# Performance work log

Hardware: AMD Instinct MI355X
Metric: run time of the kernel (lower is better)

The kernel has to match this reference:

```python
import jax, jax.numpy as jnp
import numpy as np

B, C, H, W = 32, 256, 64, 64
LN_EPS = 1e-5

def _conv1x1(x, w, b=None):
    # x: (b,c,h,w), w: (out,c) -> (b,out,h,w)
    y = jnp.einsum('bchw,oc->bohw', x, w)
    if b is not None:
        y = y + b[None, :, None, None]
    return y

def _hsigmoid(t):
    # mmcv HSigmoid: clamp((x + 3) / 6, 0, 1)
    return jnp.clip((t + 3.0) / 6.0, 0.0, 1.0)

def setup_inputs() -> dict:
    key = jax.random.key(0)
    ks = jax.random.split(key, 12)
    s = 0.05
    return {
        'x': jax.random.normal(ks[0], (B, C, H, W), jnp.float32),
        'conv0_w': jax.random.normal(ks[1], (C // 2, C), jnp.float32) * s,
        'conv0_b': jnp.zeros((C // 2,), jnp.float32),
        'bn1_w': jax.random.normal(ks[2], (C, C // 2), jnp.float32) * s,
        'bn1_b': jnp.zeros((C,), jnp.float32),
        'conv1_w': jax.random.normal(ks[3], (1, C), jnp.float32) * s,
        'conv1_b': jnp.zeros((1,), jnp.float32),
        'ln_g': jnp.ones((C,), jnp.float32),
        'ln_b': jnp.zeros((C,), jnp.float32),
        'sk_w1': jax.random.normal(ks[4], (C // 2, C), jnp.float32) * s,
        'sk_w2': jax.random.normal(ks[5], (C, C // 2), jnp.float32) * s,
        'res_w': jax.random.normal(ks[6], (C, C), jnp.float32) * s,
        'res_b': jnp.zeros((C,), jnp.float32),
    }

def reference(x, conv0_w, conv0_b, bn1_w, bn1_b, conv1_w, conv1_b,
              ln_g, ln_b, sk_w1, sk_w2, res_w, res_b):
    b, c, h, w = x.shape
    # ---- channel attention ----
    ca = _conv1x1(x, conv0_w, conv0_b)               # (b, c/2, h, w)
    ca = ca.mean(axis=(2, 3), keepdims=True)          # GAP -> (b, c/2, 1, 1)
    ca = _conv1x1(ca, bn1_w, bn1_b)                   # (b, c, 1, 1)
    ca = _hsigmoid(ca)
    v = ca.reshape(b, c)                              # nchw_to_nlc -> (b, 1, c); LN over c
    mu = v.mean(axis=-1, keepdims=True)
    var = ((v - mu) ** 2).mean(axis=-1, keepdims=True)
    v = (v - mu) * jax.lax.rsqrt(var + LN_EPS) * ln_g + ln_b
    ca = v.reshape(b, c, 1, 1)
    # ---- spatial attention ----
    sa = _conv1x1(x, conv1_w, conv1_b)                # (b, 1, h, w)
    # ---- parallel attention ----
    par = _hsigmoid(sa + ca)                          # (b, c, h, w)
    # ---- sequence attention: bmm outer product (b,c,1)x(b,1,hw) ----
    seq = _hsigmoid(ca * sa)                          # (b, c, h, w)
    # ---- SK module ----
    u = (seq + par).mean(axis=(2, 3), keepdims=True)  # GAP -> (b, c, 1, 1)
    u = _conv1x1(u, sk_w1)                            # (b, c/2, 1, 1), no bias
    u = _conv1x1(u, sk_w2)                            # (b, c, 1, 1), no bias
    a = jax.nn.softmax(u, axis=1)
    sk = seq * a + par * (1.0 - a)
    # softmax over spatial (nchw_to_nlc + Softmax(dim=1))
    sk = jax.nn.softmax(sk.reshape(b, c, h * w), axis=2).reshape(b, c, h, w)
    selected = x * sk
    # ---- self attention ----
    self_attn = selected.sum(axis=(2, 3)).reshape(b, c, 1, 1) + _conv1x1(x, res_w, res_b)
    return selected + self_attn
```

## Files before the change

### kernel.cpp

```cpp
#include <hip/hip_runtime.h>
#include <math.h>

#define B_  32
#define C_  256
#define HW_ 4096
#define LN_EPS 1e-5f

typedef __attribute__((ext_vector_type(4))) float f32x4;
typedef __attribute__((ext_vector_type(8))) short bf16x8;
typedef __attribute__((ext_vector_type(4))) unsigned u32x4;
typedef __attribute__((ext_vector_type(2))) unsigned u32x2;

__device__ __forceinline__ float hsig(float v) {
    return fminf(fmaxf((v + 3.0f) * (1.0f / 6.0f), 0.0f), 1.0f);
}
__device__ __forceinline__ float tval(float ca, float a, float sav) {
    return a * hsig(ca * sav) + (1.0f - a) * hsig(ca + sav);
}
__device__ __forceinline__ unsigned short f2bf(float f) {
    unsigned u = __float_as_uint(f);
    unsigned r = (u + 0x7fffu + ((u >> 16) & 1u)) >> 16;
    return (unsigned short)r;
}
__device__ __forceinline__ float bf2f(unsigned short h) {
    return __uint_as_float(((unsigned)h) << 16);
}
__device__ __forceinline__ int bswz(int n) {
    return ((n & 7) ^ ((n >> 3) & 7)) << 4;
}


__global__ __launch_bounds__(1024) void k_pass1c(
    const float* __restrict__ x, const float* __restrict__ w1,
    float* __restrict__ sa, float* __restrict__ xs_part,
    unsigned short* __restrict__ xbf)
{
    __shared__ float sw1[C_];
    __shared__ float sred[16][256];
    __shared__ float xsl[C_];
    int hwq = blockIdx.x, b = blockIdx.y;
    int tid = threadIdx.x, w = tid >> 6, l = tid & 63;
    int hw0 = hwq * 256;
    if (tid < 256) sw1[tid] = w1[tid];
    __syncthreads();
    const float* xb = x + (size_t)b * (C_ * HW_) + hw0 + l * 4;
    unsigned short* xo = xbf + (size_t)b * (C_ * HW_) + hw0 + l * 4;
    f32x4 sacc = {0.f, 0.f, 0.f, 0.f};
    #pragma unroll 4
    for (int i = 0; i < 16; ++i) {
        int c = i * 16 + w;
        f32x4 v = *(const f32x4*)(xb + (size_t)c * HW_);
        sacc += sw1[c] * v;
        ushort4 o = { f2bf(v.x), f2bf(v.y), f2bf(v.z), f2bf(v.w) };
        *(ushort4*)(xo + (size_t)c * HW_) = o;
        float h = (v.x + v.y) + (v.z + v.w);
        h += __shfl_xor(h, 32); h += __shfl_xor(h, 16); h += __shfl_xor(h, 8);
        h += __shfl_xor(h, 4);  h += __shfl_xor(h, 2);  h += __shfl_xor(h, 1);
        if (l == 0) xsl[c] = h;
    }
    *(f32x4*)&sred[w][l * 4] = sacc;
    __syncthreads();
    if (tid < 256) {
        float s = 0.f;
        #pragma unroll
        for (int g = 0; g < 16; ++g) s += sred[g][tid];
        sa[(size_t)b * HW_ + hw0 + tid] = s;
        xs_part[((size_t)hwq * B_ + b) * C_ + tid] = xsl[tid];
    }
}

__global__ void k_ca(const float* __restrict__ xs_part, const float* __restrict__ w0,
                     const float* __restrict__ b0, const float* __restrict__ w1,
                     const float* __restrict__ b1, const float* __restrict__ g,
                     const float* __restrict__ be, float* __restrict__ ca,
                     const float* __restrict__ rw, unsigned short* __restrict__ wbs,
                     int nparts) {
    int b = blockIdx.x, tid = threadIdx.x;
    __shared__ float xm[C_], t0[128], red[4];
    float xs = 0.f;
    for (int i = 0; i < nparts; ++i)
        xs += xs_part[((size_t)i * B_ + b) * C_ + tid];
    xm[tid] = xs * (1.0f / HW_);
    __syncthreads();
    if (tid < 128) {
        float s = b0[tid];
        const float* wr = w0 + tid * C_;
        for (int c = 0; c < C_; ++c) s += wr[c] * xm[c];
        t0[tid] = s;
    }
    __syncthreads();
    float s = b1[tid];
    const float* wr = w1 + tid * 128;
    for (int o = 0; o < 128; ++o) s += wr[o] * t0[o];
    float v = hsig(s);
    float sum = v;
    #pragma unroll
    for (int o = 32; o; o >>= 1) sum += __shfl_xor(sum, o);
    if ((tid & 63) == 0) red[tid >> 6] = sum;
    __syncthreads();
    float mu = (red[0] + red[1] + red[2] + red[3]) * (1.0f / C_);
    __syncthreads();
    float d = v - mu;
    float sq = d * d;
    #pragma unroll
    for (int o = 32; o; o >>= 1) sq += __shfl_xor(sq, o);
    if ((tid & 63) == 0) red[tid >> 6] = sq;
    __syncthreads();
    float var = (red[0] + red[1] + red[2] + red[3]) * (1.0f / C_);
    ca[b * C_ + tid] = d * (1.0f / sqrtf(var + LN_EPS)) * g[tid] + be[tid];

    int gid = b * 256 + tid;
    int lane = gid & 63;
    int mi = (gid >> 6) & 3;
    int ks = (gid >> 8) & 7;
    int wv2 = gid >> 11;
    int m = wv2 * 64 + mi * 16 + (lane & 15);
    int kb = ks * 32 + (lane >> 4) * 8;
    const float* src = rw + m * C_ + kb;
    f32x4 a4 = *(const f32x4*)src;
    f32x4 b4 = *(const f32x4*)(src + 4);
    ushort4 o0 = { f2bf(a4.x), f2bf(a4.y), f2bf(a4.z), f2bf(a4.w) };
    ushort4 o1 = { f2bf(b4.x), f2bf(b4.y), f2bf(b4.z), f2bf(b4.w) };
    unsigned short* dst = wbs + (size_t)gid * 8;
    *(ushort4*)dst = o0;
    *(ushort4*)(dst + 4) = o1;
}

__global__ void k_u(const float* __restrict__ sa, const float* __restrict__ ca,
                    const float* __restrict__ b1, float* __restrict__ u) {
    int bc = blockIdx.x;
    int b = bc >> 8;
    int tid = threadIdx.x;
    float cav = ca[bc];
    float bias = b1[0];
    const float* sp = sa + (size_t)b * HW_;
    float s = 0.f;
    for (int i = 0; i < 16; ++i) {
        f32x4 v = *(const f32x4*)(sp + i * 256 + tid * 4);
        #pragma unroll
        for (int j = 0; j < 4; ++j) {
            float sv = v[j] + bias;
            s += hsig(cav * sv) + hsig(cav + sv);
        }
    }
    #pragma unroll
    for (int o = 32; o; o >>= 1) s += __shfl_xor(s, o);
    if (tid == 0) u[bc] = s * (1.0f / HW_);
}

__global__ void k_a(const float* __restrict__ u, const float* __restrict__ w1,
                    const float* __restrict__ w2, float* __restrict__ aout) {
    int b = blockIdx.x, tid = threadIdx.x;
    __shared__ float uu[C_], v0[128], red[4];
    uu[tid] = u[b * C_ + tid];
    __syncthreads();
    if (tid < 128) {
        float s = 0.f;
        const float* wr = w1 + tid * C_;
        for (int c = 0; c < C_; ++c) s += wr[c] * uu[c];
        v0[tid] = s;
    }
    __syncthreads();
    float s = 0.f;
    const float* wr = w2 + tid * 128;
    for (int o = 0; o < 128; ++o) s += wr[o] * v0[o];
    float m = s;
    #pragma unroll
    for (int o = 32; o; o >>= 1) m = fmaxf(m, __shfl_xor(m, o));
    if ((tid & 63) == 0) red[tid >> 6] = m;
    __syncthreads();
    m = fmaxf(fmaxf(red[0], red[1]), fmaxf(red[2], red[3]));
    __syncthreads();
    float e = __expf(s - m);
    float se = e;
    #pragma unroll
    for (int o = 32; o; o >>= 1) se += __shfl_xor(se, o);
    if ((tid & 63) == 0) red[tid >> 6] = se;
    __syncthreads();
    float tot = red[0] + red[1] + red[2] + red[3];
    aout[b * C_ + tid] = e / tot;
}

__global__ void k_stats3(const unsigned short* __restrict__ xbf, const float* __restrict__ sa,
                         const float* __restrict__ b1,
                         const float* __restrict__ ca, const float* __restrict__ aw,
                         const float* __restrict__ res_b, f32x4* __restrict__ st4) {
    int bc = blockIdx.x;
    int b = bc >> 8, c = bc & 255;
    int tid = threadIdx.x;
    float cav = ca[bc], av = aw[bc];
    float bias = b1[0];
    const float* sp = sa + (size_t)b * HW_;
    const unsigned* xp = (const unsigned*)(xbf + (size_t)bc * HW_);
    float se = 0.f, xe = 0.f;
    #pragma unroll
    for (int i = 0; i < 4; ++i) {
        f32x4 s4 = *(const f32x4*)(sp + i * 1024 + tid * 4);
        u32x2 x2 = *(const u32x2*)(xp + i * 512 + tid * 2);
        float xv[4];
        xv[0] = bf2f((unsigned short)(x2[0] & 0xffffu));
        xv[1] = bf2f((unsigned short)(x2[0] >> 16));
        xv[2] = bf2f((unsigned short)(x2[1] & 0xffffu));
        xv[3] = bf2f((unsigned short)(x2[1] >> 16));
        #pragma unroll
        for (int j = 0; j < 4; ++j) {
            float e = __expf(tval(cav, av, s4[j] + bias));
            se += e;
            xe += xv[j] * e;
        }
    }
    __shared__ float red[4], red2[4];
    #pragma unroll
    for (int o = 32; o; o >>= 1) { se += __shfl_xor(se, o); xe += __shfl_xor(xe, o); }
    if ((tid & 63) == 0) { red[tid >> 6] = se; red2[tid >> 6] = xe; }
    __syncthreads();
    if (tid == 0) {
        float S = red[0] + red[1] + red[2] + red[3];
        float X = red2[0] + red2[1] + red2[2] + red2[3];
        float rcp = 1.0f / S;
        f32x4 st = { cav, av, rcp, X * rcp + res_b[c] };
        st4[bc] = st;
    }
}

__global__ __launch_bounds__(256, 3) void k_out3(
    const unsigned short* __restrict__ xbf, const unsigned short* __restrict__ wbs,
    const float* __restrict__ sa, const float* __restrict__ b1,
    const f32x4* __restrict__ st4, float* __restrict__ out)
{
    __shared__ __align__(16) unsigned short Bs[64 * 256];
    __shared__ f32x4 sst[C_];
    __shared__ float ssa[64];

    int b = blockIdx.x, tile = blockIdx.y;
    int n0 = tile * 64;
    int tid = threadIdx.x;
    int w = tid >> 6, lane = tid & 63;
    int hwc = tid & 7;
    int cq  = tid >> 3;

    const unsigned short* xb = xbf + (size_t)b * (C_ * HW_) + n0 + hwc * 8;
    u32x4 ld[2][4];
    #pragma unroll
    for (int it = 0; it < 2; ++it) {
        int c0 = it * 128 + cq * 4;
        #pragma unroll
        for (int r = 0; r < 4; ++r)
            ld[it][r] = *(const u32x4*)(xb + (size_t)(c0 + r) * HW_);
    }

    bf16x8 af[2][4];
    const bf16x8* wp = (const bf16x8*)wbs;
    #pragma unroll
    for (int ks2 = 0; ks2 < 2; ++ks2)
        #pragma unroll
        for (int mi = 0; mi < 4; ++mi)
            af[ks2][mi] = wp[(size_t)(((w * 8 + ks2) * 4 + mi) * 64 + lane)];

    sst[tid] = st4[b * C_ + tid];
    if (tid < 64) ssa[tid] = sa[(size_t)b * HW_ + n0 + tid] + b1[0];

    #pragma unroll
    for (int it = 0; it < 2; ++it) {
        int kp0 = it * 64 + cq * 2;
        #pragma unroll
        for (int e = 0; e < 8; ++e) {
            int n = hwc * 8 + e;
            unsigned a0 = ld[it][0][e >> 1], b0v = ld[it][1][e >> 1];
            unsigned a1 = ld[it][2][e >> 1], b1v = ld[it][3][e >> 1];
            unsigned d0, d1;
            if (e & 1) {
                d0 = (a0 >> 16) | (b0v & 0xffff0000u);
                d1 = (a1 >> 16) | (b1v & 0xffff0000u);
            } else {
                d0 = (a0 & 0xffffu) | (b0v << 16);
                d1 = (a1 & 0xffffu) | (b1v << 16);
            }
            int bo = (n * 512 + kp0 * 4) ^ bswz(n);
            u32x2 dd = { d0, d1 };
            *(u32x2*)((char*)Bs + bo) = dd;
        }
    }
    __syncthreads();

    f32x4 acc[4][4];
    #pragma unroll
    for (int i = 0; i < 4; ++i)
        #pragma unroll
        for (int j = 0; j < 4; ++j) acc[i][j] = (f32x4){0.f, 0.f, 0.f, 0.f};

    #pragma unroll
    for (int ksg = 0; ksg < 4; ++ksg) {
        #pragma unroll
        for (int ks2 = 0; ks2 < 2; ++ks2) {
            int ks = ksg * 2 + ks2;
            bf16x8 bfr[4];
            #pragma unroll
            for (int ni = 0; ni < 4; ++ni) {
                int n = ni * 16 + (lane & 15);
                int bo = (n * 512 + ks * 64 + (lane >> 4) * 16) ^ bswz(n);
                bfr[ni] = *(const bf16x8*)((const char*)Bs + bo);
            }
            #pragma unroll
            for (int mi = 0; mi < 4; ++mi)
                #pragma unroll
                for (int ni = 0; ni < 4; ++ni)
                    acc[mi][ni] = __builtin_amdgcn_mfma_f32_16x16x32_bf16(
                        af[ks2][mi], bfr[ni], acc[mi][ni], 0, 0, 0);
            if (ksg < 3) {
                #pragma unroll
                for (int mi = 0; mi < 4; ++mi)
                    af[ks2][mi] = wp[(size_t)(((w * 8 + (ksg + 1) * 2 + ks2) * 4 + mi) * 64 + lane)];
            }
        }
    }

    float* ob = out + (size_t)b * (C_ * HW_) + n0;
    #pragma unroll
    for (int mi = 0; mi < 4; ++mi) {
        int m0 = w * 64 + mi * 16 + (lane >> 4) * 4;
        f32x4 s0 = sst[m0 + 0];
        f32x4 s1 = sst[m0 + 1];
        f32x4 s2 = sst[m0 + 2];
        f32x4 s3 = sst[m0 + 3];
        #pragma unroll
        for (int ni = 0; ni < 4; ++ni) {
            int n = ni * 16 + (lane & 15);
            float sav = ssa[n];
            int bo = (n * 512 + m0 * 2) ^ bswz(n);
            ushort4 xv = *(const ushort4*)((const char*)Bs + bo);
            float o0 = acc[mi][ni][0] + bf2f(xv.x) * (__expf(tval(s0.x, s0.y, sav)) * s0.z) + s0.w;
            float o1 = acc[mi][ni][1] + bf2f(xv.y) * (__expf(tval(s1.x, s1.y, sav)) * s1.z) + s1.w;
            float o2 = acc[mi][ni][2] + bf2f(xv.z) * (__expf(tval(s2.x, s2.y, sav)) * s2.z) + s2.w;
            float o3 = acc[mi][ni][3] + bf2f(xv.w) * (__expf(tval(s3.x, s3.y, sav)) * s3.z) + s3.w;
            ob[(size_t)(m0 + 0) * HW_ + n] = o0;
            ob[(size_t)(m0 + 1) * HW_ + n] = o1;
            ob[(size_t)(m0 + 2) * HW_ + n] = o2;
            ob[(size_t)(m0 + 3) * HW_ + n] = o3;
        }
    }
}


__global__ void k_pass1(const float* __restrict__ x, const float* __restrict__ w1,
                        float* __restrict__ sa, float* __restrict__ xs_part)
{
    int tid = threadIdx.x, wave = tid >> 6, lane = tid & 63;
    int hwq = blockIdx.x, b = blockIdx.y, ct = blockIdx.z;
    int c0 = ct * 32;
    int hw0 = hwq * 1024;
    const float* xb = x + (size_t)b * (C_ * HW_) + hw0 + tid * 4;
    __shared__ float part[32 * 4];
    f32x4 sacc = {0.f, 0.f, 0.f, 0.f};
    #pragma unroll 4
    for (int cc = 0; cc < 32; ++cc) {
        int c = c0 + cc;
        f32x4 v = *(const f32x4*)(xb + (size_t)c * HW_);
        float wv = w1[c];
        sacc += wv * v;
        float h = (v.x + v.y) + (v.z + v.w);
        h += __shfl_xor(h, 32); h += __shfl_xor(h, 16); h += __shfl_xor(h, 8);
        h += __shfl_xor(h, 4);  h += __shfl_xor(h, 2);  h += __shfl_xor(h, 1);
        if (lane == 0) part[cc * 4 + wave] = h;
    }
    float* sp = sa + (size_t)b * HW_ + hw0 + tid * 4;
    atomicAdd(sp + 0, sacc.x);
    atomicAdd(sp + 1, sacc.y);
    atomicAdd(sp + 2, sacc.z);
    atomicAdd(sp + 3, sacc.w);
    __syncthreads();
    if (tid < 32)
        xs_part[((size_t)hwq * B_ + b) * C_ + c0 + tid] =
            part[tid * 4 + 0] + part[tid * 4 + 1] + part[tid * 4 + 2] + part[tid * 4 + 3];
}

__global__ void k_stats(const float* __restrict__ x, const float* __restrict__ sa,
                        const float* __restrict__ b1,
                        const float* __restrict__ ca, const float* __restrict__ aw,
                        const float* __restrict__ res_b, f32x4* __restrict__ st4) {
    int bc = blockIdx.x;
    int b = bc >> 8, c = bc & 255;
    int tid = threadIdx.x;
    float cav = ca[bc], av = aw[bc];
    float bias = b1[0];
    const float* sp = sa + (size_t)b * HW_;
    const float* xp = x + (size_t)bc * HW_;
    float se = 0.f, xe = 0.f;
    #pragma unroll
    for (int i = 0; i < 4; ++i) {
        f32x4 s4 = *(const f32x4*)(sp + i * 1024 + tid * 4);
        f32x4 x4 = *(const f32x4*)(xp + i * 1024 + tid * 4);
        #pragma unroll
        for (int j = 0; j < 4; ++j) {
            float e = __expf(tval(cav, av, s4[j] + bias));
            se += e;
            xe += x4[j] * e;
        }
    }
    __shared__ float red[4], red2[4];
    #pragma unroll
    for (int o = 32; o; o >>= 1) { se += __shfl_xor(se, o); xe += __shfl_xor(xe, o); }
    if ((tid & 63) == 0) { red[tid >> 6] = se; red2[tid >> 6] = xe; }
    __syncthreads();
    if (tid == 0) {
        float S = red[0] + red[1] + red[2] + red[3];
        float X = red2[0] + red2[1] + red2[2] + red2[3];
        float rcp = 1.0f / S;
        f32x4 st = { cav, av, rcp, X * rcp + res_b[c] };
        st4[bc] = st;
    }
}

__global__ __launch_bounds__(256, 2) void k_out(
    const float* __restrict__ x, const unsigned short* __restrict__ wbs,
    const float* __restrict__ sa, const float* __restrict__ b1,
    const f32x4* __restrict__ st4, float* __restrict__ out)
{
    __shared__ __align__(16) unsigned short Bs[64 * 256];
    __shared__ f32x4 sst[C_];
    __shared__ float ssa[64];

    int b = blockIdx.x, tile = blockIdx.y;
    int n0 = tile * 64;
    int tid = threadIdx.x;
    int w = tid >> 6, lane = tid & 63;

    const float* xb = x + (size_t)b * (C_ * HW_);

    bf16x8 af[8][4];
    #pragma unroll
    for (int ks = 0; ks < 8; ++ks)
        #pragma unroll
        for (int mi = 0; mi < 4; ++mi)
            af[ks][mi] = *(const bf16x8*)(wbs + (size_t)(((w * 8 + ks) * 4 + mi) * 64 + lane) * 8);

    sst[tid] = st4[b * C_ + tid];
    if (tid < 64) ssa[tid] = sa[(size_t)b * HW_ + n0 + tid] + b1[0];

    #pragma unroll
    for (int p2 = 0; p2 < 8; ++p2) {
        int id = p2 * 256 + tid;
        int kp = id >> 4;
        int tcn = id & 15;
        const float* g0 = xb + (size_t)(2 * kp) * HW_ + n0 + 4 * tcn;
        f32x4 v0 = *(const f32x4*)g0;
        f32x4 v1 = *(const f32x4*)(g0 + HW_);
        #pragma unroll
        for (int i = 0; i < 4; ++i) {
            int n = 4 * tcn + i;
            unsigned val = (unsigned)f2bf(v0[i]) | ((unsigned)f2bf(v1[i]) << 16);
            int bo = (n * 512 + kp * 4) ^ ((n & 7) << 4);
            *(unsigned*)((char*)Bs + bo) = val;
        }
    }
    __syncthreads();

    f32x4 acc[4][4];
    #pragma unroll
    for (int i = 0; i < 4; ++i)
        #pragma unroll
        for (int j = 0; j < 4; ++j) acc[i][j] = (f32x4){0.f, 0.f, 0.f, 0.f};

    #pragma unroll
    for (int ks = 0; ks < 8; ++ks) {
        bf16x8 bfr[4];
        #pragma unroll
        for (int ni = 0; ni < 4; ++ni) {
            int n = ni * 16 + (lane & 15);
            int bo = (n * 512 + ks * 64 + (lane >> 4) * 16) ^ ((n & 7) << 4);
            bfr[ni] = *(const bf16x8*)((const char*)Bs + bo);
        }
        #pragma unroll
        for (int mi = 0; mi < 4; ++mi)
            #pragma unroll
            for (int ni = 0; ni < 4; ++ni)
                acc[mi][ni] = __builtin_amdgcn_mfma_f32_16x16x32_bf16(
                    af[ks][mi], bfr[ni], acc[mi][ni], 0, 0, 0);
    }

    float* ob = out + (size_t)b * (C_ * HW_) + n0;
    #pragma unroll
    for (int mi = 0; mi < 4; ++mi) {
        int m0 = w * 64 + mi * 16 + (lane >> 4) * 4;
        f32x4 s0 = sst[m0 + 0];
        f32x4 s1 = sst[m0 + 1];
        f32x4 s2 = sst[m0 + 2];
        f32x4 s3 = sst[m0 + 3];
        #pragma unroll
        for (int ni = 0; ni < 4; ++ni) {
            int n = ni * 16 + (lane & 15);
            float sav = ssa[n];
            int bo = (n * 512 + m0 * 2) ^ ((n & 7) << 4);
            ushort4 xv = *(const ushort4*)((const char*)Bs + bo);
            float o0 = acc[mi][ni][0] + bf2f(xv.x) * (__expf(tval(s0.x, s0.y, sav)) * s0.z) + s0.w;
            float o1 = acc[mi][ni][1] + bf2f(xv.y) * (__expf(tval(s1.x, s1.y, sav)) * s1.z) + s1.w;
            float o2 = acc[mi][ni][2] + bf2f(xv.z) * (__expf(tval(s2.x, s2.y, sav)) * s2.z) + s2.w;
            float o3 = acc[mi][ni][3] + bf2f(xv.w) * (__expf(tval(s3.x, s3.y, sav)) * s3.z) + s3.w;
            ob[(size_t)(m0 + 0) * HW_ + n] = o0;
            ob[(size_t)(m0 + 1) * HW_ + n] = o1;
            ob[(size_t)(m0 + 2) * HW_ + n] = o2;
            ob[(size_t)(m0 + 3) * HW_ + n] = o3;
        }
    }
}

extern "C" void kernel_launch(void* const* d_in, const int* in_sizes, int n_in,
                              void* d_out, int out_size, void* d_ws, size_t ws_size,
                              hipStream_t stream) {
    (void)in_sizes; (void)n_in; (void)out_size;
    const float* x   = (const float*)d_in[0];
    const float* c0w = (const float*)d_in[1];
    const float* c0b = (const float*)d_in[2];
    const float* b1w = (const float*)d_in[3];
    const float* b1b = (const float*)d_in[4];
    const float* c1w = (const float*)d_in[5];
    const float* c1b = (const float*)d_in[6];
    const float* lng = (const float*)d_in[7];
    const float* lnb = (const float*)d_in[8];
    const float* sw1 = (const float*)d_in[9];
    const float* sw2 = (const float*)d_in[10];
    const float* rw  = (const float*)d_in[11];
    const float* rb  = (const float*)d_in[12];
    float* out = (float*)d_out;
    float* ws = (float*)d_ws;

    const size_t NEW_WS_FLOATS = (size_t)352256 + 16777216;
    if (ws_size >= NEW_WS_FLOATS * sizeof(float)) {
        float* sa      = ws;
        float* xs_part = ws + 131072;
        float* ca      = ws + 262144;
        float* u       = ws + 270336;
        float* aw      = ws + 278528;
        f32x4* st4     = (f32x4*)(ws + 286720);
        unsigned short* wbs = (unsigned short*)(ws + 319488);
        unsigned short* xbf = (unsigned short*)(ws + 352256);

        hipLaunchKernelGGL(k_pass1c, dim3(16, 32), dim3(1024), 0, stream, x, c1w, sa, xs_part, xbf);
        hipLaunchKernelGGL(k_ca,     dim3(32),     dim3(256), 0, stream, xs_part, c0w, c0b, b1w, b1b, lng, lnb, ca, rw, wbs, 16);
        hipLaunchKernelGGL(k_u,      dim3(8192),   dim3(64),  0, stream, sa, ca, c1b, u);
        hipLaunchKernelGGL(k_a,      dim3(32),     dim3(256), 0, stream, u, sw1, sw2, aw);
        hipLaunchKernelGGL(k_stats3, dim3(8192),   dim3(256), 0, stream, xbf, sa, c1b, ca, aw, rb, st4);
        hipLaunchKernelGGL(k_out3,   dim3(32, 64), dim3(256), 0, stream, xbf, wbs, sa, c1b, st4, out);
    } else {
        float* sa      = ws;
        float* xs_part = ws + 131072;
        float* ca      = ws + 163840;
        float* u       = ws + 172032;
        float* aw      = ws + 180224;
        f32x4* st4     = (f32x4*)(ws + 188416);
        unsigned short* wbs = (unsigned short*)(ws + 221184);

        hipMemsetAsync(sa, 0, (size_t)B_ * HW_ * sizeof(float), stream);
        hipLaunchKernelGGL(k_pass1, dim3(4, 32, 8), dim3(256), 0, stream, x, c1w, sa, xs_part);
        hipLaunchKernelGGL(k_ca,    dim3(32),       dim3(256), 0, stream, xs_part, c0w, c0b, b1w, b1b, lng, lnb, ca, rw, wbs, 4);
        hipLaunchKernelGGL(k_u,     dim3(8192),     dim3(64),  0, stream, sa, ca, c1b, u);
        hipLaunchKernelGGL(k_a,     dim3(32),       dim3(256), 0, stream, u, sw1, sw2, aw);
        hipLaunchKernelGGL(k_stats, dim3(8192),     dim3(256), 0, stream, x, sa, c1b, ca, aw, rb, st4);
        hipLaunchKernelGGL(k_out,   dim3(32, 64),   dim3(256), 0, stream, x, wbs, sa, c1b, st4, out);
    }
}
```

Before: 151.6 us.

## Split channel-sum out of first pass into separate bf16 reduction kernel

The first pass no longer computes per-channel spatial sums with wave shuffles. Each thread now handles 8 pixels with 16-byte bf16 stores, and the block covers 512 pixels. A new kernel reads the bf16 copy back to compute per-(b,c) sums, and k_ca now reads a single partial. This removes shuffle reductions from the bandwidth-bound pass, but adds a kernel launch and an extra 64MB read, and the channel sums now come from bf16-rounded values.

Result: slower. 161.7 us (+6.7%).

```diff
diff --git a/kernel.cpp b/kernel.cpp
--- a/kernel.cpp
+++ b/kernel.cpp
@@ -30,43 +30,64 @@
 }
 
 
-__global__ __launch_bounds__(1024) void k_pass1c(
+__global__ __launch_bounds__(1024) void k_pass1d(
     const float* __restrict__ x, const float* __restrict__ w1,
-    float* __restrict__ sa, float* __restrict__ xs_part,
-    unsigned short* __restrict__ xbf)
+    float* __restrict__ sa, unsigned short* __restrict__ xbf)
 {
     __shared__ float sw1[C_];
-    __shared__ float sred[16][256];
-    __shared__ float xsl[C_];
+    __shared__ float sred[16][512];
     int hwq = blockIdx.x, b = blockIdx.y;
     int tid = threadIdx.x, w = tid >> 6, l = tid & 63;
-    int hw0 = hwq * 256;
+    int hw0 = hwq * 512;
     if (tid < 256) sw1[tid] = w1[tid];
     __syncthreads();
-    const float* xb = x + (size_t)b * (C_ * HW_) + hw0 + l * 4;
-    unsigned short* xo = xbf + (size_t)b * (C_ * HW_) + hw0 + l * 4;
-    f32x4 sacc = {0.f, 0.f, 0.f, 0.f};
+    const float* xb = x + (size_t)b * (C_ * HW_) + hw0 + l * 8;
+    unsigned short* xo = xbf + (size_t)b * (C_ * HW_) + hw0 + l * 8;
+    f32x4 s0 = {0.f, 0.f, 0.f, 0.f}, s1 = {0.f, 0.f, 0.f, 0.f};
     #pragma unroll 4
     for (int i = 0; i < 16; ++i) {
         int c = i * 16 + w;
-        f32x4 v = *(const f32x4*)(xb + (size_t)c * HW_);
-        sacc += sw1[c] * v;
-        ushort4 o = { f2bf(v.x), f2bf(v.y), f2bf(v.z), f2bf(v.w) };
-        *(ushort4*)(xo + (size_t)c * HW_) = o;
-        float h = (v.x + v.y) + (v.z + v.w);
-        h += __shfl_xor(h, 32); h += __shfl_xor(h, 16); h += __shfl_xor(h, 8);
-        h += __shfl_xor(h, 4);  h += __shfl_xor(h, 2);  h += __shfl_xor(h, 1);
-        if (l == 0) xsl[c] = h;
-    }
-    *(f32x4*)&sred[w][l * 4] = sacc;
-    __syncthreads();
-    if (tid < 256) {
+        const float* p = xb + (size_t)c * HW_;
+        f32x4 v0 = *(const f32x4*)p;
+        f32x4 v1 = *(const f32x4*)(p + 4);
+        float wv = sw1[c];
+        s0 += wv * v0;
+        s1 += wv * v1;
+        u32x4 o;
+        o[0] = (unsigned)f2bf(v0.x) | ((unsigned)f2bf(v0.y) << 16);
+        o[1] = (unsigned)f2bf(v0.z) | ((unsigned)f2bf(v0.w) << 16);
+        o[2] = (unsigned)f2bf(v1.x) | ((unsigned)f2bf(v1.y) << 16);
+        o[3] = (unsigned)f2bf(v1.z) | ((unsigned)f2bf(v1.w) << 16);
+        *(u32x4*)(xo + (size_t)c * HW_) = o;
+    }
+    *(f32x4*)&sred[w][l * 8] = s0;
+    *(f32x4*)&sred[w][l * 8 + 4] = s1;
+    __syncthreads();
+    if (tid < 512) {
         float s = 0.f;
         #pragma unroll
         for (int g = 0; g < 16; ++g) s += sred[g][tid];
         sa[(size_t)b * HW_ + hw0 + tid] = s;
-        xs_part[((size_t)hwq * B_ + b) * C_ + tid] = xsl[tid];
-    }
+    }
+}
+
+__global__ void k_xs(const unsigned short* __restrict__ xbf, float* __restrict__ xs) {
+    int bc = blockIdx.x;
+    int l = threadIdx.x;
+    const u32x4* p = (const u32x4*)(xbf + (size_t)bc * HW_);
+    float s = 0.f;
+    #pragma unroll
+    for (int i = 0; i < 8; ++i) {
+        u32x4 v = p[i * 64 + l];
+        #pragma unroll
+        for (int j = 0; j < 4; ++j) {
+            s += bf2f((unsigned short)(v[j] & 0xffffu));
+            s += bf2f((unsigned short)(v[j] >> 16));
+        }
+    }
+    #pragma unroll
+    for (int o = 32; o; o >>= 1) s += __shfl_xor(s, o);
+    if (l == 0) xs[bc] = s;
 }
 
 __global__ void k_ca(const float* __restrict__ xs_part, const float* __restrict__ w0,
@@ -535,12 +556,13 @@
         unsigned short* wbs = (unsigned short*)(ws + 319488);
         unsigned short* xbf = (unsigned short*)(ws + 352256);
 
-        hipLaunchKernelGGL(k_pass1c, dim3(16, 32), dim3(1024), 0, stream, x, c1w, sa, xs_part, xbf);
-        hipLaunchKernelGGL(k_ca,     dim3(32),     dim3(256), 0, stream, xs_part, c0w, c0b, b1w, b1b, lng, lnb, ca, rw, wbs, 16);
-        hipLaunchKernelGGL(k_u,      dim3(8192),   dim3(64),  0, stream, sa, ca, c1b, u);
-        hipLaunchKernelGGL(k_a,      dim3(32),     dim3(256), 0, stream, u, sw1, sw2, aw);
-        hipLaunchKernelGGL(k_stats3, dim3(8192),   dim3(256), 0, stream, xbf, sa, c1b, ca, aw, rb, st4);
-        hipLaunchKernelGGL(k_out3,   dim3(32, 64), dim3(256), 0, stream, xbf, wbs, sa, c1b, st4, out);
+        hipLaunchKernelGGL(k_pass1d, dim3(8, 32),  dim3(1024), 0, stream, x, c1w, sa, xbf);
+        hipLaunchKernelGGL(k_xs,     dim3(8192),   dim3(64),   0, stream, xbf, xs_part);
+        hipLaunchKernelGGL(k_ca,     dim3(32),     dim3(256),  0, stream, xs_part, c0w, c0b, b1w, b1b, lng, lnb, ca, rw, wbs, 1);
+        hipLaunchKernelGGL(k_u,      dim3(8192),   dim3(64),   0, stream, sa, ca, c1b, u);
+        hipLaunchKernelGGL(k_a,      dim3(32),     dim3(256),  0, stream, u, sw1, sw2, aw);
+        hipLaunchKernelGGL(k_stats3, dim3(8192),   dim3(256),  0, stream, xbf, sa, c1b, ca, aw, rb, st4);
+        hipLaunchKernelGGL(k_out3,   dim3(32, 64), dim3(256),  0, stream, xbf, wbs, sa, c1b, st4, out);
     } else {
         float* sa      = ws;
         float* xs_part = ws + 131072;
```
